# Kernel tuning notes

Hardware: AMD Instinct MI355X
Metric: run time of the kernel (lower is better)

## Reference

```python
import jax, jax.numpy as jnp
import numpy as np

N_Q = 32      # questions per batch
N_DOCS = 8    # docs per question (positive first)
Q_LEN = 32    # query tokens
D_LEN = 200   # doc tokens
DIM = 128     # ColBERT embedding dim


def setup_inputs() -> dict:
    key = jax.random.key(0)
    k1, k2 = jax.random.split(key)
    hq = jax.random.normal(k1, (N_Q, Q_LEN, DIM), dtype=jnp.float32)
    hd = jax.random.normal(k2, (N_Q * N_DOCS, D_LEN, DIM), dtype=jnp.float32)
    return {"hq": hq, "hd": hd}


def reference(hq, hd):
    # ColBERT maxsim: [n, m, q, d] token-level scores
    scores = jnp.einsum("nqh,mdh->nmqd", hq, hd)
    # max over doc tokens, mean over query tokens -> [n, m]
    score_matrix = jnp.max(scores, axis=-1).mean(axis=-1)

    n, m = score_matrix.shape
    n_docs = m // n
    # positive doc is the first in each group: targets = [0, n_docs, 2*n_docs, ...]
    targets = jnp.arange(0, m, n_docs)
    logp = jax.nn.log_softmax(score_matrix, axis=-1)
    loss = -jnp.mean(jnp.take_along_axis(logp, targets[:, None], axis=1))
    return score_matrix, loss
```

## Files before the change

kernel.cpp:

```cpp
#include <hip/hip_runtime.h>
#include <hip/hip_bf16.h>
#include <math.h>

typedef short short8 __attribute__((ext_vector_type(8)));
typedef float f32x4 __attribute__((ext_vector_type(4)));

#define NQ 32
#define NDOCS 8
#define QLEN 32
#define DLEN 200
#define DIM 128
#define MD 256
#define HD_ROWS 208
#define DOC_SHORTS (HD_ROWS * DIM)
#define DOC_BYTES (DOC_SHORTS * 2)
#define DOC_CHUNKS (HD_ROWS * 16)

__device__ __forceinline__ short f2bf(float x) {
    union { float f; unsigned u; } v; v.f = x;
    unsigned r = v.u + 0x7FFFu + ((v.u >> 16) & 1u);
    return (short)(r >> 16);
}

__device__ __forceinline__ short8 cvt8(float4 f0, float4 f1) {
    short8 o;
    o[0] = f2bf(f0.x); o[1] = f2bf(f0.y); o[2] = f2bf(f0.z); o[3] = f2bf(f0.w);
    o[4] = f2bf(f1.x); o[5] = f2bf(f1.y); o[6] = f2bf(f1.z); o[7] = f2bf(f1.w);
    return o;
}

__global__ __launch_bounds__(256) void convert_hd(const float* __restrict__ hd,
                                                  short* __restrict__ hdb) {
    unsigned c = blockIdx.x * 256 + threadIdx.x;
    unsigned m = c / DOC_CHUNKS;
    unsigned rc = c - m * DOC_CHUNKS;
    unsigned row = rc >> 4, kc = rc & 15;
    short8 o = {0, 0, 0, 0, 0, 0, 0, 0};
    if (row < DLEN) {
        const float4* p = reinterpret_cast<const float4*>(
            hd + ((size_t)m * DLEN + row) * DIM + kc * 8);
        o = cvt8(p[0], p[1]);
    }
    unsigned dst = m * DOC_CHUNKS + row * 16 + (kc ^ (row & 7));
    reinterpret_cast<short8*>(hdb)[dst] = o;
}

__global__ __launch_bounds__(512, 2) void colbert_scores(const float* __restrict__ hq,
                                                         const short* __restrict__ hdb,
                                                         float* __restrict__ out) {
    __shared__ char lds[DOC_BYTES];
    const int tid = threadIdx.x;
    const int b = blockIdx.x;
    const int m = b & 255, qh = b >> 8;
    const int wid = tid >> 6, lane = tid & 63;
    const int lg = lane >> 4, lr = lane & 15;
    const int n0 = qh * 16 + wid * 2;

    const char* gsrc = reinterpret_cast<const char*>(hdb + (size_t)m * DOC_SHORTS);
    {
        const int lbase = wid * 1024;
        const int gbase = lbase + lane * 16;
        #pragma unroll
        for (int i = 0; i < 6; ++i)
            __builtin_amdgcn_global_load_lds(
                (const __attribute__((address_space(1))) void*)(gsrc + i * 8192 + gbase),
                (__attribute__((address_space(3))) void*)(lds + i * 8192 + lbase),
                16, 0, 0);
        if (wid < 4)
            __builtin_amdgcn_global_load_lds(
                (const __attribute__((address_space(1))) void*)(gsrc + 49152 + gbase),
                (__attribute__((address_space(3))) void*)(lds + 49152 + lbase),
                16, 0, 0);
    }

    short8 Bq[2][2][4];
    #pragma unroll
    for (int nn = 0; nn < 2; ++nn)
        #pragma unroll
        for (int qt = 0; qt < 2; ++qt)
            #pragma unroll
            for (int s = 0; s < 4; ++s) {
                const float4* p = reinterpret_cast<const float4*>(
                    hq + (size_t)((n0 + nn) * QLEN + qt * 16 + lr) * DIM + s * 32 + lg * 8);
                Bq[nn][qt][s] = cvt8(p[0], p[1]);
            }

    __syncthreads();

    int va[4];
    #pragma unroll
    for (int s = 0; s < 4; ++s)
        va[s] = lr * 256 + ((s * 64 + lg * 16) ^ ((lr & 7) << 4));

    float qmax[2][2];
    #pragma unroll
    for (int nn = 0; nn < 2; ++nn)
        #pragma unroll
        for (int qt = 0; qt < 2; ++qt) qmax[nn][qt] = -INFINITY;

#define STEP(DT, MASKED)                                                          \
    {                                                                             \
        f32x4 a00 = {0,0,0,0}, a01 = {0,0,0,0}, a10 = {0,0,0,0}, a11 = {0,0,0,0}; \
        __builtin_amdgcn_s_setprio(1);                                            \
        _Pragma("unroll")                                                         \
        for (int s = 0; s < 4; ++s) {                                             \
            short8 A_ = *reinterpret_cast<const short8*>(&lds[va[s] + (DT) * 4096]); \
            a00 = __builtin_amdgcn_mfma_f32_16x16x32_bf16(A_, Bq[0][0][s], a00, 0, 0, 0); \
            a01 = __builtin_amdgcn_mfma_f32_16x16x32_bf16(A_, Bq[0][1][s], a01, 0, 0, 0); \
            a10 = __builtin_amdgcn_mfma_f32_16x16x32_bf16(A_, Bq[1][0][s], a10, 0, 0, 0); \
            a11 = __builtin_amdgcn_mfma_f32_16x16x32_bf16(A_, Bq[1][1][s], a11, 0, 0, 0); \
        }                                                                         \
        __builtin_amdgcn_s_setprio(0);                                            \
        if (!(MASKED) || lg < 2) {                                                \
            qmax[0][0] = fmaxf(qmax[0][0], fmaxf(fmaxf(a00[0], a00[1]), fmaxf(a00[2], a00[3]))); \
            qmax[0][1] = fmaxf(qmax[0][1], fmaxf(fmaxf(a01[0], a01[1]), fmaxf(a01[2], a01[3]))); \
            qmax[1][0] = fmaxf(qmax[1][0], fmaxf(fmaxf(a10[0], a10[1]), fmaxf(a10[2], a10[3]))); \
            qmax[1][1] = fmaxf(qmax[1][1], fmaxf(fmaxf(a11[0], a11[1]), fmaxf(a11[2], a11[3]))); \
        }                                                                         \
    }

    #pragma unroll
    for (int dt = 0; dt < 12; ++dt) STEP(dt, false);
    STEP(12, true);
#undef STEP

    #pragma unroll
    for (int off = 16; off <= 32; off <<= 1)
        #pragma unroll
        for (int nn = 0; nn < 2; ++nn)
            #pragma unroll
            for (int qt = 0; qt < 2; ++qt)
                qmax[nn][qt] = fmaxf(qmax[nn][qt], __shfl_xor(qmax[nn][qt], off, 64));

    float s0 = qmax[0][0] + qmax[0][1];
    float s1 = qmax[1][0] + qmax[1][1];
    #pragma unroll
    for (int off = 1; off <= 8; off <<= 1) {
        s0 += __shfl_xor(s0, off, 64);
        s1 += __shfl_xor(s1, off, 64);
    }
    if (lane == 0) {
        out[(size_t)n0 * MD + m] = s0 * (1.0f / 32.0f);
        out[(size_t)(n0 + 1) * MD + m] = s1 * (1.0f / 32.0f);
    }
}

__global__ __launch_bounds__(256) void colbert_loss(const float* __restrict__ scores,
                                                    float* __restrict__ loss_out) {
    __shared__ float terms[NQ];
    const int tid = threadIdx.x;
    const int wid = tid >> 6, lane = tid & 63;
    for (int n = wid; n < NQ; n += 4) {
        const float* row = scores + n * MD;
        float v0 = row[lane], v1 = row[64 + lane], v2 = row[128 + lane], v3 = row[192 + lane];
        float mx = fmaxf(fmaxf(v0, v1), fmaxf(v2, v3));
        #pragma unroll
        for (int off = 1; off < 64; off <<= 1) mx = fmaxf(mx, __shfl_xor(mx, off, 64));
        float s = expf(v0 - mx) + expf(v1 - mx) + expf(v2 - mx) + expf(v3 - mx);
        #pragma unroll
        for (int off = 1; off < 64; off <<= 1) s += __shfl_xor(s, off, 64);
        if (lane == 0) terms[n] = (mx + logf(s)) - row[n * NDOCS];
    }
    __syncthreads();
    if (tid == 0) {
        float acc = 0.f;
        #pragma unroll
        for (int n = 0; n < NQ; ++n) acc += terms[n];
        loss_out[0] = acc * (1.0f / NQ);
    }
}

extern "C" void kernel_launch(void* const* d_in, const int* in_sizes, int n_in,
                              void* d_out, int out_size, void* d_ws, size_t ws_size,
                              hipStream_t stream) {
    const float* hq = (const float*)d_in[0];
    const float* hd = (const float*)d_in[1];
    float* out = (float*)d_out;
    short* hdb = (short*)d_ws;

    convert_hd<<<3328, 256, 0, stream>>>(hd, hdb);
    colbert_scores<<<512, 512, 0, stream>>>(hq, hdb, out);
    colbert_loss<<<1, 256, 0, stream>>>(out, out + NQ * MD);
}
```

Measured before the change: 46.44 us.

## Fuse fp32-to-bf16 doc conversion into scores kernel and halve block size

Removes the separate conversion kernel and workspace: each scores block now loads the fp32 document directly, converts it to bf16 and writes a swizzled tile into LDS. Blocks shrink to 256 threads covering 8 questions each, with twice as many blocks, and the setprio hints are dropped. This saves a launch and a workspace round trip but multiplies fp32 document reads across blocks and replaces async global-to-LDS loads with register-staged conversion.

```diff
diff --git a/kernel.cpp b/kernel.cpp
--- a/kernel.cpp
+++ b/kernel.cpp
@@ -11,10 +11,7 @@
 #define DLEN 200
 #define DIM 128
 #define MD 256
-#define HD_ROWS 208
-#define DOC_SHORTS (HD_ROWS * DIM)
-#define DOC_BYTES (DOC_SHORTS * 2)
-#define DOC_CHUNKS (HD_ROWS * 16)
+#define ROWB 256
 
 __device__ __forceinline__ short f2bf(float x) {
     union { float f; unsigned u; } v; v.f = x;
@@ -29,48 +26,34 @@
     return o;
 }
 
-__global__ __launch_bounds__(256) void convert_hd(const float* __restrict__ hd,
-                                                  short* __restrict__ hdb) {
-    unsigned c = blockIdx.x * 256 + threadIdx.x;
-    unsigned m = c / DOC_CHUNKS;
-    unsigned rc = c - m * DOC_CHUNKS;
-    unsigned row = rc >> 4, kc = rc & 15;
-    short8 o = {0, 0, 0, 0, 0, 0, 0, 0};
-    if (row < DLEN) {
-        const float4* p = reinterpret_cast<const float4*>(
-            hd + ((size_t)m * DLEN + row) * DIM + kc * 8);
-        o = cvt8(p[0], p[1]);
-    }
-    unsigned dst = m * DOC_CHUNKS + row * 16 + (kc ^ (row & 7));
-    reinterpret_cast<short8*>(hdb)[dst] = o;
+__device__ __forceinline__ void writeChunk(char* lds, int c, float4 f0, float4 f1) {
+    int row = c >> 4, kc = c & 15;
+    int byte = row * ROWB + ((kc * 16) ^ ((row & 7) << 4));
+    *reinterpret_cast<short8*>(&lds[byte]) = cvt8(f0, f1);
 }
 
-__global__ __launch_bounds__(512, 2) void colbert_scores(const float* __restrict__ hq,
-                                                         const short* __restrict__ hdb,
+__global__ __launch_bounds__(256, 2) void colbert_scores(const float* __restrict__ hq,
+                                                         const float* __restrict__ hd,
                                                          float* __restrict__ out) {
-    __shared__ char lds[DOC_BYTES];
+    __shared__ char lds[208 * ROWB];
     const int tid = threadIdx.x;
     const int b = blockIdx.x;
-    const int m = b & 255, qh = b >> 8;
+    const int m = b & 255, qo = b >> 8;
     const int wid = tid >> 6, lane = tid & 63;
     const int lg = lane >> 4, lr = lane & 15;
-    const int n0 = qh * 16 + wid * 2;
+    const int n0 = qo * 8 + wid * 2;
 
-    const char* gsrc = reinterpret_cast<const char*>(hdb + (size_t)m * DOC_SHORTS);
-    {
-        const int lbase = wid * 1024;
-        const int gbase = lbase + lane * 16;
-        #pragma unroll
-        for (int i = 0; i < 6; ++i)
-            __builtin_amdgcn_global_load_lds(
-                (const __attribute__((address_space(1))) void*)(gsrc + i * 8192 + gbase),
-                (__attribute__((address_space(3))) void*)(lds + i * 8192 + lbase),
-                16, 0, 0);
-        if (wid < 4)
-            __builtin_amdgcn_global_load_lds(
-                (const __attribute__((address_space(1))) void*)(gsrc + 49152 + gbase),
-                (__attribute__((address_space(3))) void*)(lds + 49152 + lbase),
-                16, 0, 0);
+    const float4* src4 = reinterpret_cast<const float4*>(hd + (size_t)m * (DLEN * DIM));
+    #pragma unroll
+    for (int i = 0; i < 12; ++i) {
+        int c = tid + i * 256;
+        float4 f0 = src4[c * 2], f1 = src4[c * 2 + 1];
+        writeChunk(lds, c, f0, f1);
+    }
+    if (tid < 128) {
+        int c = 3072 + tid;
+        float4 f0 = src4[c * 2], f1 = src4[c * 2 + 1];
+        writeChunk(lds, c, f0, f1);
     }
 
     short8 Bq[2][2][4];
@@ -90,7 +73,7 @@
     int va[4];
     #pragma unroll
     for (int s = 0; s < 4; ++s)
-        va[s] = lr * 256 + ((s * 64 + lg * 16) ^ ((lr & 7) << 4));
+        va[s] = lr * ROWB + ((s * 64 + lg * 16) ^ ((lr & 7) << 4));
 
     float qmax[2][2];
     #pragma unroll
@@ -101,7 +84,6 @@
 #define STEP(DT, MASKED)                                                          \
     {                                                                             \
         f32x4 a00 = {0,0,0,0}, a01 = {0,0,0,0}, a10 = {0,0,0,0}, a11 = {0,0,0,0}; \
-        __builtin_amdgcn_s_setprio(1);                                            \
         _Pragma("unroll")                                                         \
         for (int s = 0; s < 4; ++s) {                                             \
             short8 A_ = *reinterpret_cast<const short8*>(&lds[va[s] + (DT) * 4096]); \
@@ -110,7 +92,6 @@
             a10 = __builtin_amdgcn_mfma_f32_16x16x32_bf16(A_, Bq[1][0][s], a10, 0, 0, 0); \
             a11 = __builtin_amdgcn_mfma_f32_16x16x32_bf16(A_, Bq[1][1][s], a11, 0, 0, 0); \
         }                                                                         \
-        __builtin_amdgcn_s_setprio(0);                                            \
         if (!(MASKED) || lg < 2) {                                                \
             qmax[0][0] = fmaxf(qmax[0][0], fmaxf(fmaxf(a00[0], a00[1]), fmaxf(a00[2], a00[3]))); \
             qmax[0][1] = fmaxf(qmax[0][1], fmaxf(fmaxf(a01[0], a01[1]), fmaxf(a01[2], a01[3]))); \
@@ -176,9 +157,7 @@
     const float* hq = (const float*)d_in[0];
     const float* hd = (const float*)d_in[1];
     float* out = (float*)d_out;
-    short* hdb = (short*)d_ws;
 
-    convert_hd<<<3328, 256, 0, stream>>>(hd, hdb);
-    colbert_scores<<<512, 512, 0, stream>>>(hq, hdb, out);
+    colbert_scores<<<1024, 256, 0, stream>>>(hq, hd, out);
     colbert_loss<<<1, 256, 0, stream>>>(out, out + NQ * MD);
 }
```

Measured after the change: 39.71 us. 14.5% less time.
